# Kernel tuning notes

Measured on AMD Instinct MI355X. Metric: run time of the kernel, lower is better.

Reference implementation:

```python
import jax, jax.numpy as jnp
import numpy as np

HIDDEN = 2048
NUM_Q_HEADS = 16
NUM_KV_HEADS = 4
HEAD_DIM = HIDDEN // NUM_Q_HEADS  # 128
KV_REP = NUM_Q_HEADS // NUM_KV_HEADS  # 4
KV_DIM = HEAD_DIM * NUM_KV_HEADS


def setup_inputs() -> dict:
    key = jax.random.key(0)
    ks = jax.random.split(key, 9)
    B, S = 2, 2048
    s_in = 1.0 / np.sqrt(HIDDEN)
    return {
        "hidden_states": jax.random.normal(ks[0], (B, S, HIDDEN), dtype=jnp.float32),
        "Wq": jax.random.normal(ks[1], (HIDDEN, HIDDEN), dtype=jnp.float32) * s_in,
        "bq": jnp.zeros((HIDDEN,), dtype=jnp.float32),
        "Wk": jax.random.normal(ks[2], (HIDDEN, KV_DIM), dtype=jnp.float32) * s_in,
        "bk": jnp.zeros((KV_DIM,), dtype=jnp.float32),
        "Wv": jax.random.normal(ks[3], (HIDDEN, KV_DIM), dtype=jnp.float32) * s_in,
        "bv": jnp.zeros((KV_DIM,), dtype=jnp.float32),
        "Wo": jax.random.normal(ks[4], (HIDDEN, HIDDEN), dtype=jnp.float32) * s_in,
        "bo": jnp.zeros((HIDDEN,), dtype=jnp.float32),
    }


def reference(hidden_states, Wq, bq, Wk, bk, Wv, bv, Wo, bo):
    B, S, H = hidden_states.shape
    # projections
    q = hidden_states @ Wq + bq  # [B,S,H]
    k = hidden_states @ Wk + bk  # [B,S,KV_DIM]
    v = hidden_states @ Wv + bv  # [B,S,KV_DIM]
    # [B, heads, S, head_dim]
    q = q.reshape(B, S, NUM_Q_HEADS, HEAD_DIM).transpose(0, 2, 1, 3)
    k = k.reshape(B, S, NUM_KV_HEADS, HEAD_DIM).transpose(0, 2, 1, 3)
    v = v.reshape(B, S, NUM_KV_HEADS, HEAD_DIM).transpose(0, 2, 1, 3)
    # repeat_interleave KV heads to match q heads
    k = jnp.repeat(k, KV_REP, axis=1)  # [B,Hq,S,hd]
    v = jnp.repeat(v, KV_REP, axis=1)
    scale = 1.0 / np.sqrt(HEAD_DIM)
    scores = jnp.einsum('bhqd,bhkd->bhqk', q, k) * scale  # [B,Hq,S,S]
    causal = jnp.triu(jnp.ones((S, S), dtype=bool), k=1)
    scores = jnp.where(causal[None, None], -jnp.inf, scores)
    probs = jax.nn.softmax(scores, axis=-1)
    ctx = jnp.einsum('bhqk,bhkd->bhqd', probs, v)  # [B,Hq,S,hd]
    ctx = ctx.transpose(0, 2, 1, 3).reshape(B, S, H)
    return ctx @ Wo + bo
```

## Files before the change

kernel.cpp:

```cpp
#include <hip/hip_runtime.h>
#include <hip/hip_bf16.h>
#include <stdint.h>

#define SEQ 2048
#define BATCH 2
#define NTOK (SEQ * BATCH)
#define HID 2048
#define NQH 16
#define NKVH 4
#define HD 128
#define KVD 512

typedef __bf16 bf16x8 __attribute__((ext_vector_type(8)));
typedef float f32x4 __attribute__((ext_vector_type(4)));
typedef float f32x16 __attribute__((ext_vector_type(16)));
typedef unsigned int u32;

__device__ __forceinline__ unsigned short f2bf(float f) {
    uint32_t u = __builtin_bit_cast(uint32_t, f);
    uint32_t r = (u + 0x7fffu + ((u >> 16) & 1u)) >> 16;
    return (unsigned short)r;
}

__device__ __forceinline__ u32 cvtpk(float lo, float hi) {
    u32 r;
    asm("v_cvt_pk_bf16_f32 %0, %1, %2" : "=v"(r) : "v"(lo), "v"(hi));
    return r;
}

__device__ __forceinline__ void gload16(const void* g, void* l) {
    __builtin_amdgcn_global_load_lds((const __attribute__((address_space(1))) u32*)g,
                                     (__attribute__((address_space(3))) u32*)l, 16, 0, 0);
}

__global__ void cvt_f32_bf16(const float* __restrict__ in, unsigned short* __restrict__ out, int n4) {
    int i = blockIdx.x * blockDim.x + threadIdx.x;
    int stride = gridDim.x * blockDim.x;
    for (; i < n4; i += stride) {
        float4 v = ((const float4*)in)[i];
        ushort4 o;
        o.x = f2bf(v.x); o.y = f2bf(v.y); o.z = f2bf(v.z); o.w = f2bf(v.w);
        ((ushort4*)out)[i] = o;
    }
}

__global__ __launch_bounds__(256) void transpose_w(const float* __restrict__ W,
                                                   unsigned short* __restrict__ Wt, int N) {
    __shared__ unsigned short tile[64][72];
    const int k0 = blockIdx.x * 64, n0 = blockIdx.y * 64;
    const int t = threadIdx.x;
    const int r = t >> 4;
    const int c4 = (t & 15) * 4;
    #pragma unroll
    for (int i = 0; i < 4; i++) {
        int row = r + i * 16;
        float4 v = *(const float4*)&W[(size_t)(k0 + row) * N + n0 + c4];
        tile[row][c4 + 0] = f2bf(v.x);
        tile[row][c4 + 1] = f2bf(v.y);
        tile[row][c4 + 2] = f2bf(v.z);
        tile[row][c4 + 3] = f2bf(v.w);
    }
    __syncthreads();
    #pragma unroll
    for (int i = 0; i < 4; i++) {
        int nrow = r + i * 16;
        ushort4 o;
        o.x = tile[c4 + 0][nrow];
        o.y = tile[c4 + 1][nrow];
        o.z = tile[c4 + 2][nrow];
        o.w = tile[c4 + 3][nrow];
        *(ushort4*)&Wt[(size_t)(n0 + nrow) * HID + k0 + c4] = o;
    }
}

template <int MODE>
__global__ __launch_bounds__(256) void gemm_tn(const unsigned short* __restrict__ A,
                                               const unsigned short* __restrict__ Bt,
                                               const float* __restrict__ bias,
                                               const float* __restrict__ bias2,
                                               void* __restrict__ out1,
                                               void* __restrict__ out2) {
    __shared__ unsigned short Asm[2][128 * 64];
    __shared__ unsigned short Bsm[2][128 * 64];
    const int m0 = blockIdx.x * 128;
    const int n0 = blockIdx.y * 128;
    const int t = threadIdx.x;
    const int lane = t & 63, w = t >> 6;
    const int wr = (w >> 1) * 64, wc = (w & 1) * 64;
    const int l16 = lane & 15, lg = lane >> 4;

    f32x4 acc[4][4] = {};

    auto stage = [&](int buf, int kt) {
        const int k0 = kt * 64;
        #pragma unroll
        for (int it = 0; it < 4; it++) {
            int base = it * 256 + w * 64;
            int qc = base + lane;
            int row = qc >> 3, c = qc & 7;
            int col = ((c ^ (row & 7)) << 3);
            gload16(&A[(size_t)(m0 + row) * HID + k0 + col], (char*)&Asm[buf][0] + base * 16);
            gload16(&Bt[(size_t)(n0 + row) * HID + k0 + col], (char*)&Bsm[buf][0] + base * 16);
        }
    };

    stage(0, 0);
    __syncthreads();
    int buf = 0;
    for (int kt = 0; kt < HID / 64; kt++) {
        if (kt < HID / 64 - 1) stage(buf ^ 1, kt + 1);
        const char* Ab = (const char*)&Asm[buf][0];
        const char* Bb = (const char*)&Bsm[buf][0];
        #pragma unroll
        for (int kk = 0; kk < 2; kk++) {
            bf16x8 af[4], bfr[4];
            #pragma unroll
            for (int m = 0; m < 4; m++) {
                int row = wr + m * 16 + l16;
                af[m] = *(const bf16x8*)(Ab + row * 128 + (((kk * 4 + lg) ^ (row & 7)) << 4));
            }
            #pragma unroll
            for (int n = 0; n < 4; n++) {
                int row = wc + n * 16 + l16;
                bfr[n] = *(const bf16x8*)(Bb + row * 128 + (((kk * 4 + lg) ^ (row & 7)) << 4));
            }
            #pragma unroll
            for (int m = 0; m < 4; m++)
                #pragma unroll
                for (int n = 0; n < 4; n++)
                    acc[m][n] = __builtin_amdgcn_mfma_f32_16x16x32_bf16(af[m], bfr[n], acc[m][n], 0, 0, 0);
        }
        __syncthreads();
        buf ^= 1;
    }
    #pragma unroll
    for (int m = 0; m < 4; m++) {
        int row = m0 + wr + m * 16 + lg * 4;
        #pragma unroll
        for (int n = 0; n < 4; n++) {
            int col = n0 + wc + n * 16 + l16;
            #pragma unroll
            for (int r = 0; r < 4; r++) {
                float v = acc[m][n][r];
                int rr = row + r;
                if constexpr (MODE == 0) {
                    v = (v + bias[col]) * 0.08838834764831845f;
                    ((unsigned short*)out1)[(size_t)rr * HID + col] = f2bf(v);
                } else if constexpr (MODE == 1) {
                    if (col < 512) {
                        v += bias[col];
                        ((unsigned short*)out1)[(size_t)rr * KVD + col] = f2bf(v);
                    } else {
                        int c2 = col - 512;
                        v += bias2[c2];
                        int b = rr >> 11, s = rr & (SEQ - 1);
                        ((unsigned short*)out2)[((size_t)b * KVD + c2) * SEQ + s] = f2bf(v);
                    }
                } else {
                    v += bias[col];
                    ((float*)out1)[(size_t)rr * HID + col] = v;
                }
            }
        }
    }
}

__global__ __launch_bounds__(256, 2) void attn(const unsigned short* __restrict__ Q,
                                               const unsigned short* __restrict__ K,
                                               const unsigned short* __restrict__ Vt,
                                               unsigned short* __restrict__ ctx) {
    __shared__ unsigned short Ksm[2][64 * 128];
    __shared__ unsigned short Vsm[2][128 * 64];
    const int n = blockIdx.x;
    const int qx = n & 15;
    const int qt = (n < 256) ? (15 - qx) : qx;
    const int bh = (n >> 4) & 31;
    const int b = bh >> 4, h = bh & 15, hk = h >> 2;
    const int t = threadIdx.x, w = t >> 6, lane = t & 63;
    const int lam = lane & 31, hi = lane >> 5;
    const int qw = qt * 128 + w * 32;
    const int qg = qw + lam;
    const size_t qrowbase = (size_t)b * SEQ + qw;

    const unsigned short* Kg = K + (size_t)b * SEQ * KVD + hk * HD;
    const unsigned short* Vg = Vt + ((size_t)b * KVD + hk * HD) * SEQ;

    bf16x8 qf[8];
    #pragma unroll
    for (int kc = 0; kc < 8; kc++)
        qf[kc] = *(const bf16x8*)&Q[(qrowbase + lam) * HID + h * HD + kc * 16 + hi * 8];

    f32x16 oacc[4] = {};
    float m = -1e30f, l = 0.f;

    auto stage = [&](int buf, int kt) {
        const int kvb = kt * 64;
        #pragma unroll
        for (int it = 0; it < 4; it++) {
            int base = it * 256 + w * 64;
            int qc = base + lane;
            {
                int row = qc >> 4, c = qc & 15;
                gload16(&Kg[(size_t)(kvb + row) * KVD + ((c ^ (row & 7)) << 3)],
                        (char*)&Ksm[buf][0] + base * 16);
            }
            {
                int row = qc >> 3, c = qc & 7;
                gload16(&Vg[(size_t)row * SEQ + kvb + ((c ^ (row & 7)) << 3)],
                        (char*)&Vsm[buf][0] + base * 16);
            }
        }
    };

    const int ntile = 2 * qt + 2;
    stage(0, 0);
    __syncthreads();
    int buf = 0;
    for (int kt = 0; kt < ntile; kt++) {
        const int kvb = kt * 64;
        if (kt + 1 < ntile) stage(buf ^ 1, kt + 1);
        if (kvb <= qw + 31) {
            const char* Kb = (const char*)&Ksm[buf][0];
            const char* Vb = (const char*)&Vsm[buf][0];
            f32x16 st0 = {}, st1 = {};
            #pragma unroll
            for (int kc = 0; kc < 8; kc++) {
                int coff = (kc * 32 + hi * 16) ^ ((lam & 7) << 4);
                bf16x8 kf0 = *(const bf16x8*)(Kb + lam * 256 + coff);
                bf16x8 kf1 = *(const bf16x8*)(Kb + (32 + lam) * 256 + coff);
                st0 = __builtin_amdgcn_mfma_f32_32x32x16_bf16(kf0, qf[kc], st0, 0, 0, 0);
                st1 = __builtin_amdgcn_mfma_f32_32x32x16_bf16(kf1, qf[kc], st1, 0, 0, 0);
            }
            if (kvb + 63 > qw) {
                #pragma unroll
                for (int r = 0; r < 16; r++) {
                    int krow = (r & 3) + 8 * (r >> 2) + 4 * hi;
                    if (kvb + krow > qg) st0[r] = -1e30f;
                    if (kvb + 32 + krow > qg) st1[r] = -1e30f;
                }
            }
            float tmax = st0[0];
            #pragma unroll
            for (int r = 1; r < 16; r++) tmax = fmaxf(tmax, st0[r]);
            #pragma unroll
            for (int r = 0; r < 16; r++) tmax = fmaxf(tmax, st1[r]);
            tmax = fmaxf(tmax, __shfl_xor(tmax, 32));
            float mn = fmaxf(m, tmax);
            float sf = __expf(m - mn);
            m = mn;
            float rs = 0.f;
            #pragma unroll
            for (int r = 0; r < 16; r++) { st0[r] = __expf(st0[r] - mn); rs += st0[r]; }
            #pragma unroll
            for (int r = 0; r < 16; r++) { st1[r] = __expf(st1[r] - mn); rs += st1[r]; }
            rs += __shfl_xor(rs, 32);
            l = l * sf + rs;
            #pragma unroll
            for (int dc = 0; dc < 4; dc++)
                #pragma unroll
                for (int r = 0; r < 16; r++) oacc[dc][r] *= sf;
            u32 pw0[4][2], pw1[4][2];
            #pragma unroll
            for (int g = 0; g < 4; g++) {
                pw0[g][0] = cvtpk(st0[4 * g], st0[4 * g + 1]);
                pw0[g][1] = cvtpk(st0[4 * g + 2], st0[4 * g + 3]);
                pw1[g][0] = cvtpk(st1[4 * g], st1[4 * g + 1]);
                pw1[g][1] = cvtpk(st1[4 * g + 2], st1[4 * g + 3]);
            }
            #pragma unroll
            for (int kc = 0; kc < 4; kc++) {
                const u32 (*pw)[2] = (kc >> 1) ? pw1 : pw0;
                int g0 = (kc & 1) * 2;
                u32 own0 = hi ? pw[g0 + 1][0] : pw[g0][0];
                u32 own1 = hi ? pw[g0 + 1][1] : pw[g0][1];
                u32 off0 = hi ? pw[g0][0] : pw[g0 + 1][0];
                u32 off1 = hi ? pw[g0][1] : pw[g0 + 1][1];
                u32 xw0 = __shfl_xor(off0, 32);
                u32 xw1 = __shfl_xor(off1, 32);
                int4 paw;
                paw.x = hi ? xw0 : own0;
                paw.y = hi ? xw1 : own1;
                paw.z = hi ? own0 : xw0;
                paw.w = hi ? own1 : xw1;
                bf16x8 pa = __builtin_bit_cast(bf16x8, paw);
                #pragma unroll
                for (int dc = 0; dc < 4; dc++) {
                    bf16x8 vf = *(const bf16x8*)(Vb + (dc * 32 + lam) * 128 +
                                                 ((kc * 32 + hi * 16) ^ ((lam & 7) << 4)));
                    oacc[dc] = __builtin_amdgcn_mfma_f32_32x32x16_bf16(vf, pa, oacc[dc], 0, 0, 0);
                }
            }
        }
        __syncthreads();
        buf ^= 1;
    }

    float inv = 1.f / l;
    char* osm = (char*)&Ksm[0][0] + w * 8192;
    #pragma unroll
    for (int dc = 0; dc < 4; dc++)
        #pragma unroll
        for (int r = 0; r < 16; r += 2) {
            int d = dc * 32 + (r & 3) + 8 * (r >> 2) + 4 * hi;
            u32 wd = cvtpk(oacc[dc][r] * inv, oacc[dc][r + 1] * inv);
            *(u32*)(osm + lam * 256 + ((d * 2) ^ ((lam & 7) << 4))) = wd;
        }
    __syncthreads();
    const int q2 = lane >> 1, half = lane & 1;
    #pragma unroll
    for (int cc = 0; cc < 8; cc++) {
        bf16x8 v = *(const bf16x8*)(osm + q2 * 256 + (((half * 8 + cc) * 16) ^ ((q2 & 7) << 4)));
        *(bf16x8*)&ctx[(qrowbase + q2) * HID + h * HD + half * 64 + cc * 8] = v;
    }
}

extern "C" void kernel_launch(void* const* d_in, const int* in_sizes, int n_in,
                              void* d_out, int out_size, void* d_ws, size_t ws_size,
                              hipStream_t stream) {
    const float* X  = (const float*)d_in[0];
    const float* Wq = (const float*)d_in[1];
    const float* bq = (const float*)d_in[2];
    const float* Wk = (const float*)d_in[3];
    const float* bk = (const float*)d_in[4];
    const float* Wv = (const float*)d_in[5];
    const float* bv = (const float*)d_in[6];
    const float* Wo = (const float*)d_in[7];
    const float* bo = (const float*)d_in[8];
    float* out = (float*)d_out;

    const size_t MB = 1u << 20;
    char* ws = (char*)d_ws;
    if (ws_size < 76 * MB) return;
    unsigned short* Xb   = (unsigned short*)(ws + 0 * MB);
    unsigned short* Wqt  = (unsigned short*)(ws + 16 * MB);
    unsigned short* Wkvt = (unsigned short*)(ws + 24 * MB);
    unsigned short* Wot  = (unsigned short*)(ws + 28 * MB);
    unsigned short* Qb   = (unsigned short*)(ws + 36 * MB);
    unsigned short* Kb   = (unsigned short*)(ws + 52 * MB);
    unsigned short* Vtb  = (unsigned short*)(ws + 56 * MB);
    unsigned short* Ctx  = (unsigned short*)(ws + 60 * MB);

    cvt_f32_bf16<<<2048, 256, 0, stream>>>(X, Xb, NTOK * HID / 4);
    transpose_w<<<dim3(HID / 64, HID / 64), 256, 0, stream>>>(Wq, Wqt, HID);
    transpose_w<<<dim3(HID / 64, KVD / 64), 256, 0, stream>>>(Wk, Wkvt, KVD);
    transpose_w<<<dim3(HID / 64, KVD / 64), 256, 0, stream>>>(Wv, Wkvt + (size_t)512 * HID, KVD);
    transpose_w<<<dim3(HID / 64, HID / 64), 256, 0, stream>>>(Wo, Wot, HID);

    gemm_tn<0><<<dim3(NTOK / 128, HID / 128), 256, 0, stream>>>(Xb, Wqt, bq, nullptr, Qb, nullptr);
    gemm_tn<1><<<dim3(NTOK / 128, 1024 / 128), 256, 0, stream>>>(Xb, Wkvt, bk, bv, Kb, Vtb);

    attn<<<dim3(512), 256, 0, stream>>>(Qb, Kb, Vtb, Ctx);

    gemm_tn<3><<<dim3(NTOK / 128, HID / 128), 256, 0, stream>>>(Ctx, Wot, bo, nullptr, out, nullptr);
}
```

Measured before the change: 230.5 us.

## Fuse QKV projection into one 256x256-tiled pipelined GEMM and merge weight transposes

Result: slower. 237.7 us (+3.1%).

```diff
diff --git a/kernel.cpp b/kernel.cpp
--- a/kernel.cpp
+++ b/kernel.cpp
@@ -10,6 +10,7 @@
 #define NKVH 4
 #define HD 128
 #define KVD 512
+#define NT 32
 
 typedef __bf16 bf16x8 __attribute__((ext_vector_type(8)));
 typedef float f32x4 __attribute__((ext_vector_type(4)));
@@ -44,10 +45,22 @@
     }
 }
 
-__global__ __launch_bounds__(256) void transpose_w(const float* __restrict__ W,
-                                                   unsigned short* __restrict__ Wt, int N) {
+__global__ __launch_bounds__(256) void transpose_all(const float* __restrict__ Wq,
+                                                     const float* __restrict__ Wk,
+                                                     const float* __restrict__ Wv,
+                                                     const float* __restrict__ Wo,
+                                                     unsigned short* __restrict__ Wqkvt,
+                                                     unsigned short* __restrict__ Wot) {
     __shared__ unsigned short tile[64][72];
-    const int k0 = blockIdx.x * 64, n0 = blockIdx.y * 64;
+    const int y = blockIdx.y;
+    const float* W;
+    unsigned short* dst;
+    int N, ny;
+    if (y < 32)      { W = Wq; dst = Wqkvt;                        N = 2048; ny = y; }
+    else if (y < 40) { W = Wk; dst = Wqkvt + (size_t)2048 * HID;   N = 512;  ny = y - 32; }
+    else if (y < 48) { W = Wv; dst = Wqkvt + (size_t)2560 * HID;   N = 512;  ny = y - 40; }
+    else             { W = Wo; dst = Wot;                          N = 2048; ny = y - 48; }
+    const int k0 = blockIdx.x * 64, n0 = ny * 64;
     const int t = threadIdx.x;
     const int r = t >> 4;
     const int c4 = (t & 15) * 4;
@@ -69,7 +82,159 @@
         o.y = tile[c4 + 1][nrow];
         o.z = tile[c4 + 2][nrow];
         o.w = tile[c4 + 3][nrow];
-        *(ushort4*)&Wt[(size_t)(n0 + nrow) * HID + k0 + c4] = o;
+        *(ushort4*)&dst[(size_t)(n0 + nrow) * HID + k0 + c4] = o;
+    }
+}
+
+__global__ __launch_bounds__(512, 1) void gemm_qkv(const unsigned short* __restrict__ A,
+                                                   const unsigned short* __restrict__ Bt,
+                                                   const float* __restrict__ bq,
+                                                   const float* __restrict__ bk,
+                                                   const float* __restrict__ bv,
+                                                   unsigned short* __restrict__ Qo,
+                                                   unsigned short* __restrict__ Ko,
+                                                   unsigned short* __restrict__ Vo) {
+    __shared__ __align__(16) unsigned short AL[2][2][256 * 32];
+    __shared__ __align__(16) unsigned short BL[2][2][256 * 32];
+    const int m0 = blockIdx.x * 256;
+    const int nb = blockIdx.y;
+    const int n0 = nb * 256;
+    const int tid = threadIdx.x;
+    const int lane = tid & 63, w = tid >> 6;
+    const int wm = w >> 2, wn = w & 3;
+    const int l16 = lane & 15, lg = lane >> 4;
+
+    f32x4 acc[8][4] = {};
+
+    auto stageHT = [&](int ts, int ht) {
+        if (ts >= NT) return;
+        const int kh = ht >> 1;
+        const int k0 = ts * 64 + kh * 32;
+        const unsigned short* src = (ht & 1) ? Bt + (size_t)n0 * HID : A + (size_t)m0 * HID;
+        char* dstBase = (char*)((ht & 1) ? &BL[ts & 1][kh][0] : &AL[ts & 1][kh][0]);
+        #pragma unroll
+        for (int j = 0; j < 2; j++) {
+            int ch = j * 512 + tid;
+            int row = ch >> 2, slot = ch & 3;
+            int cg = slot ^ ((row >> 1) & 3);
+            gload16(&src[(size_t)row * HID + k0 + cg * 8], dstBase + (j * 512 + w * 64) * 16);
+        }
+    };
+    auto readA = [&](const unsigned short* base, int mh, int mf) -> bf16x8 {
+        int row = wm * 128 + mh * 64 + mf * 16 + l16;
+        return *(const bf16x8*)((const char*)base + row * 64 + ((lg ^ ((row >> 1) & 3)) << 4));
+    };
+    auto readB = [&](const unsigned short* base, int nf) -> bf16x8 {
+        int row = wn * 64 + nf * 16 + l16;
+        return *(const bf16x8*)((const char*)base + row * 64 + ((lg ^ ((row >> 1) & 3)) << 4));
+    };
+
+    stageHT(0, 0); stageHT(0, 1); stageHT(0, 2); stageHT(0, 3);
+    stageHT(1, 0); stageHT(1, 1);
+
+    for (int t = 0; t < NT; t++) {
+        const int buf = t & 1;
+        const unsigned short* A0 = &AL[buf][0][0];
+        const unsigned short* A1 = &AL[buf][1][0];
+        const unsigned short* B0 = &BL[buf][0][0];
+        const unsigned short* B1 = &BL[buf][1][0];
+        const int h = 4 * t + 6;
+        bf16x8 af[4], bfr[4];
+
+        stageHT(h >> 2, h & 3);
+        if (t == NT - 1) { asm volatile("s_waitcnt vmcnt(0)" ::: "memory"); }
+        else             { asm volatile("s_waitcnt vmcnt(6)" ::: "memory"); }
+        __builtin_amdgcn_s_barrier();
+        __builtin_amdgcn_sched_barrier(0);
+        #pragma unroll
+        for (int mf = 0; mf < 4; mf++) af[mf] = readA(A0, 0, mf);
+        #pragma unroll
+        for (int nf = 0; nf < 4; nf++) bfr[nf] = readB(B0, nf);
+        asm volatile("s_waitcnt lgkmcnt(0)" ::: "memory");
+        __builtin_amdgcn_sched_barrier(0);
+        __builtin_amdgcn_s_setprio(1);
+        #pragma unroll
+        for (int mf = 0; mf < 4; mf++)
+            #pragma unroll
+            for (int nf = 0; nf < 4; nf++)
+                acc[mf][nf] = __builtin_amdgcn_mfma_f32_16x16x32_bf16(af[mf], bfr[nf], acc[mf][nf], 0, 0, 0);
+        __builtin_amdgcn_s_setprio(0);
+        __builtin_amdgcn_s_barrier();
+
+        #pragma unroll
+        for (int mf = 0; mf < 4; mf++) af[mf] = readA(A0, 1, mf);
+        stageHT((h + 1) >> 2, (h + 1) & 3);
+        __builtin_amdgcn_s_barrier();
+        asm volatile("s_waitcnt lgkmcnt(0)" ::: "memory");
+        __builtin_amdgcn_sched_barrier(0);
+        __builtin_amdgcn_s_setprio(1);
+        #pragma unroll
+        for (int mf = 0; mf < 4; mf++)
+            #pragma unroll
+            for (int nf = 0; nf < 4; nf++)
+                acc[4 + mf][nf] = __builtin_amdgcn_mfma_f32_16x16x32_bf16(af[mf], bfr[nf], acc[4 + mf][nf], 0, 0, 0);
+        __builtin_amdgcn_s_setprio(0);
+        __builtin_amdgcn_s_barrier();
+
+        #pragma unroll
+        for (int mf = 0; mf < 4; mf++) af[mf] = readA(A1, 0, mf);
+        #pragma unroll
+        for (int nf = 0; nf < 4; nf++) bfr[nf] = readB(B1, nf);
+        stageHT((h + 2) >> 2, (h + 2) & 3);
+        __builtin_amdgcn_s_barrier();
+        asm volatile("s_waitcnt lgkmcnt(0)" ::: "memory");
+        __builtin_amdgcn_sched_barrier(0);
+        __builtin_amdgcn_s_setprio(1);
+        #pragma unroll
+        for (int mf = 0; mf < 4; mf++)
+            #pragma unroll
+            for (int nf = 0; nf < 4; nf++)
+                acc[mf][nf] = __builtin_amdgcn_mfma_f32_16x16x32_bf16(af[mf], bfr[nf], acc[mf][nf], 0, 0, 0);
+        __builtin_amdgcn_s_setprio(0);
+        __builtin_amdgcn_s_barrier();
+
+        #pragma unroll
+        for (int mf = 0; mf < 4; mf++) af[mf] = readA(A1, 1, mf);
+        stageHT((h + 3) >> 2, (h + 3) & 3);
+        __builtin_amdgcn_s_barrier();
+        asm volatile("s_waitcnt lgkmcnt(0)" ::: "memory");
+        __builtin_amdgcn_sched_barrier(0);
+        __builtin_amdgcn_s_setprio(1);
+        #pragma unroll
+        for (int mf = 0; mf < 4; mf++)
+            #pragma unroll
+            for (int nf = 0; nf < 4; nf++)
+                acc[4 + mf][nf] = __builtin_amdgcn_mfma_f32_16x16x32_bf16(af[mf], bfr[nf], acc[4 + mf][nf], 0, 0, 0);
+        __builtin_amdgcn_s_setprio(0);
+        __builtin_amdgcn_s_barrier();
+    }
+
+    const float sc = 0.08838834764831845f;
+    #pragma unroll
+    for (int am = 0; am < 8; am++) {
+        int row = m0 + wm * 128 + (am >> 2) * 64 + (am & 3) * 16 + lg * 4;
+        #pragma unroll
+        for (int nf = 0; nf < 4; nf++) {
+            int col = n0 + wn * 64 + nf * 16 + l16;
+            #pragma unroll
+            for (int r = 0; r < 4; r++) {
+                float v = acc[am][nf][r];
+                int rr = row + r;
+                if (nb < 8) {
+                    v = (v + bq[col]) * sc;
+                    Qo[(size_t)rr * HID + col] = f2bf(v);
+                } else if (nb < 10) {
+                    int c = col - 2048;
+                    v += bk[c];
+                    Ko[(size_t)rr * KVD + c] = f2bf(v);
+                } else {
+                    int c = col - 2560;
+                    v += bv[c];
+                    int b = rr >> 11, s = rr & (SEQ - 1);
+                    Vo[((size_t)b * KVD + c) * SEQ + s] = f2bf(v);
+                }
+            }
+        }
     }
 }
 
@@ -77,9 +242,7 @@
 __global__ __launch_bounds__(256) void gemm_tn(const unsigned short* __restrict__ A,
                                                const unsigned short* __restrict__ Bt,
                                                const float* __restrict__ bias,
-                                               const float* __restrict__ bias2,
-                                               void* __restrict__ out1,
-                                               void* __restrict__ out2) {
+                                               void* __restrict__ out1) {
     __shared__ unsigned short Asm[2][128 * 64];
     __shared__ unsigned short Bsm[2][128 * 64];
     const int m0 = blockIdx.x * 128;
@@ -141,25 +304,8 @@
             int col = n0 + wc + n * 16 + l16;
             #pragma unroll
             for (int r = 0; r < 4; r++) {
-                float v = acc[m][n][r];
-                int rr = row + r;
-                if constexpr (MODE == 0) {
-                    v = (v + bias[col]) * 0.08838834764831845f;
-                    ((unsigned short*)out1)[(size_t)rr * HID + col] = f2bf(v);
-                } else if constexpr (MODE == 1) {
-                    if (col < 512) {
-                        v += bias[col];
-                        ((unsigned short*)out1)[(size_t)rr * KVD + col] = f2bf(v);
-                    } else {
-                        int c2 = col - 512;
-                        v += bias2[c2];
-                        int b = rr >> 11, s = rr & (SEQ - 1);
-                        ((unsigned short*)out2)[((size_t)b * KVD + c2) * SEQ + s] = f2bf(v);
-                    }
-                } else {
-                    v += bias[col];
-                    ((float*)out1)[(size_t)rr * HID + col] = v;
-                }
+                float v = acc[m][n][r] + bias[col];
+                ((float*)out1)[(size_t)(row + r) * HID + col] = v;
             }
         }
     }
@@ -172,9 +318,8 @@
     __shared__ unsigned short Ksm[2][64 * 128];
     __shared__ unsigned short Vsm[2][128 * 64];
     const int n = blockIdx.x;
-    const int qx = n & 15;
-    const int qt = (n < 256) ? (15 - qx) : qx;
-    const int bh = (n >> 4) & 31;
+    const int qt = 15 - (n >> 5);
+    const int bh = n & 31;
     const int b = bh >> 4, h = bh & 15, hk = h >> 2;
     const int t = threadIdx.x, w = t >> 6, lane = t & 63;
     const int lam = lane & 31, hi = lane >> 5;
@@ -331,25 +476,20 @@
     const size_t MB = 1u << 20;
     char* ws = (char*)d_ws;
     if (ws_size < 76 * MB) return;
-    unsigned short* Xb   = (unsigned short*)(ws + 0 * MB);
-    unsigned short* Wqt  = (unsigned short*)(ws + 16 * MB);
-    unsigned short* Wkvt = (unsigned short*)(ws + 24 * MB);
-    unsigned short* Wot  = (unsigned short*)(ws + 28 * MB);
-    unsigned short* Qb   = (unsigned short*)(ws + 36 * MB);
-    unsigned short* Kb   = (unsigned short*)(ws + 52 * MB);
-    unsigned short* Vtb  = (unsigned short*)(ws + 56 * MB);
-    unsigned short* Ctx  = (unsigned short*)(ws + 60 * MB);
+    unsigned short* Xb    = (unsigned short*)(ws + 0 * MB);
+    unsigned short* Wqkvt = (unsigned short*)(ws + 16 * MB);
+    unsigned short* Wot   = (unsigned short*)(ws + 28 * MB);
+    unsigned short* Qb    = (unsigned short*)(ws + 36 * MB);
+    unsigned short* Kb    = (unsigned short*)(ws + 52 * MB);
+    unsigned short* Vtb   = (unsigned short*)(ws + 56 * MB);
+    unsigned short* Ctx   = (unsigned short*)(ws + 60 * MB);
 
     cvt_f32_bf16<<<2048, 256, 0, stream>>>(X, Xb, NTOK * HID / 4);
-    transpose_w<<<dim3(HID / 64, HID / 64), 256, 0, stream>>>(Wq, Wqt, HID);
-    transpose_w<<<dim3(HID / 64, KVD / 64), 256, 0, stream>>>(Wk, Wkvt, KVD);
-    transpose_w<<<dim3(HID / 64, KVD / 64), 256, 0, stream>>>(Wv, Wkvt + (size_t)512 * HID, KVD);
-    transpose_w<<<dim3(HID / 64, HID / 64), 256, 0, stream>>>(Wo, Wot, HID);
-
-    gemm_tn<0><<<dim3(NTOK / 128, HID / 128), 256, 0, stream>>>(Xb, Wqt, bq, nullptr, Qb, nullptr);
-    gemm_tn<1><<<dim3(NTOK / 128, 1024 / 128), 256, 0, stream>>>(Xb, Wkvt, bk, bv, Kb, Vtb);
+    transpose_all<<<dim3(32, 80), 256, 0, stream>>>(Wq, Wk, Wv, Wo, Wqkvt, Wot);
+
+    gemm_qkv<<<dim3(16, 12), 512, 0, stream>>>(Xb, Wqkvt, bq, bk, bv, Qb, Kb, Vtb);
 
     attn<<<dim3(512), 256, 0, stream>>>(Qb, Kb, Vtb, Ctx);
 
-    gemm_tn<3><<<dim3(NTOK / 128, HID / 128), 256, 0, stream>>>(Ctx, Wot, bo, nullptr, out, nullptr);
-}
+    gemm_tn<3><<<dim3(NTOK / 128, HID / 128), 256, 0, stream>>>(Ctx, Wot, bo, (void*)out);
+}
```
